# Optimization experiments

Hardware: AMD Instinct MI355X
Metric: run time of the kernel (lower is better)

Reference implementation:

```python
import jax, jax.numpy as jnp
import numpy as np

ROPE_THETA = 500000.0


def apply_rope(x, position_ids):
    # x: (B, H, S, hd), position_ids: (B, S)
    hd = x.shape[-1]
    inv_freq = 1.0 / (ROPE_THETA ** (jnp.arange(0, hd, 2, dtype=x.dtype) / hd))  # (hd/2,)
    freqs = position_ids.astype(x.dtype)[:, :, None] * inv_freq  # (B, S, hd/2)
    sin = jnp.sin(freqs)[:, None, :, :]  # (B, 1, S, hd/2)
    cos = jnp.cos(freqs)[:, None, :, :]
    x1 = x[..., ::2]
    x2 = x[..., 1::2]
    even = x1 * cos - x2 * sin
    odd = x2 * cos + x1 * sin
    # interleave even/odd back: stack on a new trailing axis then flatten
    return jnp.stack([even, odd], axis=-1).reshape(x.shape)


def setup_inputs() -> dict:
    key = jax.random.key(0)
    k_x, k_q, k_k, k_v, k_o = jax.random.split(key, 5)
    B, S, D = 2, 2048, 2048
    H, H_kv = 32, 8
    hd = D // H
    x = jax.random.normal(k_x, (B, S, D), dtype=jnp.float32)
    position_ids = jnp.broadcast_to(jnp.arange(S, dtype=jnp.int64)[None, :], (B, S))
    scale = 0.02
    Wq = jax.random.normal(k_q, (D, H * hd), dtype=jnp.float32) * scale
    Wk = jax.random.normal(k_k, (D, H_kv * hd), dtype=jnp.float32) * scale
    Wv = jax.random.normal(k_v, (D, H_kv * hd), dtype=jnp.float32) * scale
    Wo = jax.random.normal(k_o, (D, D), dtype=jnp.float32) * scale
    return {"x": x, "position_ids": position_ids, "Wq": Wq, "Wk": Wk, "Wv": Wv, "Wo": Wo}


def reference(x, position_ids, Wq, Wk, Wv, Wo):
    B, S, D = x.shape
    H, H_kv = 32, 8
    hd = D // H
    G = H // H_kv  # query heads per kv head

    q = (x @ Wq).reshape(B, S, H, hd).transpose(0, 2, 1, 3)        # (B, H, S, hd)
    k = (x @ Wk).reshape(B, S, H_kv, hd).transpose(0, 2, 1, 3)     # (B, H_kv, S, hd)
    v = (x @ Wv).reshape(B, S, H_kv, hd).transpose(0, 2, 1, 3)

    q = apply_rope(q, position_ids)
    k = apply_rope(k, position_ids)

    # GQA: group query heads (B, H_kv, G, S, hd); repeat_interleave maps head h -> kv head h // G
    qg = q.reshape(B, H_kv, G, S, hd)
    scores = jnp.einsum("bkgsh,bkth->bkgst", qg, k) / jnp.sqrt(jnp.asarray(hd, x.dtype))

    causal = jnp.triu(jnp.ones((S, S), dtype=bool), 1)  # True = masked
    scores = jnp.where(causal, jnp.asarray(-jnp.inf, scores.dtype), scores)

    attn = jax.nn.softmax(scores, axis=-1)  # (B, H_kv, G, S, S)
    z = jnp.einsum("bkgst,bkth->bkgsh", attn, v)  # (B, H_kv, G, S, hd)
    z = z.reshape(B, H, S, hd).transpose(0, 2, 1, 3).reshape(B, S, D)
    return z @ Wo
```

## Files before the change

### kernel.cpp

```cpp
#include <hip/hip_runtime.h>
#include <hip/hip_bf16.h>


#define S_LEN 2048
#define DIM   2048
#define NH    32
#define NKV   8
#define HD    64
#define BS    4096
#define NQKV  3072
#define LL(x) ((long long)(x))

typedef __bf16 bf16x8 __attribute__((ext_vector_type(8)));
typedef float  f32x4  __attribute__((ext_vector_type(4)));
typedef float  f32x16 __attribute__((ext_vector_type(16)));
typedef unsigned u32x4 __attribute__((ext_vector_type(4)));

__device__ __forceinline__ unsigned short bfb(float f) {
  __hip_bfloat16 h = __float2bfloat16(f);
  return *reinterpret_cast<unsigned short*>(&h);
}

__device__ __forceinline__ unsigned cvtpk(float lo, float hi) {
  unsigned u;
  asm("v_cvt_pk_bf16_f32 %0, %1, %2" : "=v"(u) : "v"(lo), "v"(hi));
  return u;
}

__device__ __forceinline__ void gload16(const void* g, void* l) {
  __builtin_amdgcn_global_load_lds(
      (const __attribute__((address_space(1))) void*)g,
      (__attribute__((address_space(3))) void*)l, 16, 0, 0);
}

__device__ __forceinline__ void tcast_body(
    const float* __restrict__ in, unsigned short* __restrict__ out,
    int K, int N, int bx, int by, int tid, float* tile ) {
  int n0 = bx * 32, k0 = by * 32;
  int tx = tid & 31, ty = tid >> 5;
#pragma unroll
  for (int r = 0; r < 32; r += 8)
    tile[(ty + r) * 33 + tx] = in[LL(k0 + ty + r) * N + n0 + tx];
  __syncthreads();
#pragma unroll
  for (int r = 0; r < 32; r += 8)
    out[LL(n0 + ty + r) * K + k0 + tx] = bfb(tile[tx * 33 + ty + r]);
}

__global__ __launch_bounds__(256) void k_prep(
    const float* __restrict__ x,  const float* __restrict__ Wq,
    const float* __restrict__ Wk, const float* __restrict__ Wv,
    const float* __restrict__ Wo, float* __restrict__ tab,
    unsigned short* __restrict__ xb, unsigned short* __restrict__ wqkvt,
    unsigned short* __restrict__ wot) {
  __shared__ float tile[32 * 33];
  int blk = blockIdx.x, tid = threadIdx.x;
  if (blk < 256) {
    int i = blk * 256 + tid;
    int s = i >> 5, f = i & 31;
    double inv = pow(500000.0, -2.0 * (double)f / 64.0);
    double fr = (double)s * inv;
    tab[2 * i]     = (float)cos(fr);
    tab[2 * i + 1] = (float)sin(fr);
  } else if (blk < 8448) {
    int i = (blk - 256) * 256 + tid;
    float4 v = ((const float4*)x)[i];
    ushort4 o;
    o.x = bfb(v.x); o.y = bfb(v.y); o.z = bfb(v.z); o.w = bfb(v.w);
    ((ushort4*)xb)[i] = o;
  } else if (blk < 12544) {
    int t2 = blk - 8448;
    tcast_body(Wq, wqkvt, DIM, DIM, t2 & 63, t2 >> 6, tid, tile);
  } else if (blk < 13568) {
    int t3 = blk - 12544;
    tcast_body(Wk, wqkvt + LL(2048) * DIM, DIM, 512, t3 & 15, t3 >> 4, tid, tile);
  } else if (blk < 14592) {
    int t4 = blk - 13568;
    tcast_body(Wv, wqkvt + LL(2560) * DIM, DIM, 512, t4 & 15, t4 >> 4, tid, tile);
  } else {
    int t5 = blk - 14592;
    tcast_body(Wo, wot, DIM, DIM, t5 & 63, t5 >> 6, tid, tile);
  }
}

template <int MODE>
__global__ __launch_bounds__(256, 2) void k_gemm(
    const unsigned short* __restrict__ A, const unsigned short* __restrict__ Bt,
    void* __restrict__ Cout, int M, int N, int K,
    const float* __restrict__ tab, unsigned short* __restrict__ qbuf,
    unsigned short* __restrict__ kbuf, unsigned short* __restrict__ vtb) {
  __shared__ __align__(16) unsigned short As[128 * 32];
  __shared__ __align__(16) unsigned short Bs[128 * 32];
  int t = threadIdx.x;
  int lane = t & 63, w = t >> 6;
  int wr = w >> 1, wc = w & 1;
  int g = lane >> 4, r = lane & 15;
  int gx = gridDim.x;
  int nwg = gx * gridDim.y;
  int lin = blockIdx.y * gx + blockIdx.x;
  int cpx = nwg >> 3;
  int swz = (lin & 7) * cpx + (lin >> 3);
  int bx = swz % gx, by = swz / gx;
  long long rowBase = LL(by) * 128;
  long long colBase = LL(bx) * 128;

  f32x4 acc[4][4] = {};

  int c0 = t, c1 = t + 256;
  const unsigned short* ag0 = A + (rowBase + (c0 >> 2)) * K + (c0 & 3) * 8;
  const unsigned short* ag1 = A + (rowBase + (c1 >> 2)) * K + (c1 & 3) * 8;
  const unsigned short* bg0 = Bt + (colBase + (c0 >> 2)) * K + (c0 & 3) * 8;
  const unsigned short* bg1 = Bt + (colBase + (c1 >> 2)) * K + (c1 & 3) * 8;
  char* lA0 = (char*)As + c0 * 16; char* lA1 = (char*)As + c1 * 16;
  char* lB0 = (char*)Bs + c0 * 16; char* lB1 = (char*)Bs + c1 * 16;

  for (int kt = 0; kt < K; kt += 32) {
    __syncthreads();
    gload16(ag0 + kt, lA0);
    gload16(ag1 + kt, lA1);
    gload16(bg0 + kt, lB0);
    gload16(bg1 + kt, lB1);
    __syncthreads();

    bf16x8 af[4], bfr[4];
#pragma unroll
    for (int m = 0; m < 4; m++)
      af[m] = *(const bf16x8*)(const void*)(As + (wr * 64 + m * 16 + r) * 32 + g * 8);
#pragma unroll
    for (int n = 0; n < 4; n++)
      bfr[n] = *(const bf16x8*)(const void*)(Bs + (wc * 64 + n * 16 + r) * 32 + g * 8);
#pragma unroll
    for (int m = 0; m < 4; m++)
#pragma unroll
      for (int n = 0; n < 4; n++)
        acc[m][n] = __builtin_amdgcn_mfma_f32_16x16x32_bf16(af[m], bfr[n], acc[m][n], 0, 0, 0);
  }

  if (MODE == 0) {
#pragma unroll
    for (int m = 0; m < 4; m++)
#pragma unroll
      for (int n = 0; n < 4; n++) {
        long long row0 = rowBase + wr * 64 + m * 16 + g * 4;
        long long col = colBase + wc * 64 + n * 16 + r;
#pragma unroll
        for (int j = 0; j < 4; j++)
          ((float*)Cout)[(row0 + j) * N + col] = acc[m][n][j];
      }
  } else {
#pragma unroll
    for (int n = 0; n < 4; n++) {
      int gc0 = (int)colBase + wc * 64 + n * 16;
      int gc = gc0 + r;
      if (gc0 < 2560) {
        unsigned short* dst; int dcol, dstride; float scale;
        if (gc0 < 2048) { dst = qbuf; dcol = gc;        dstride = DIM; scale = 0.18033688f; }
        else            { dst = kbuf; dcol = gc - 2048; dstride = 512; scale = 1.0f; }
        int f = (gc & 63) >> 1;
        float sgn = (gc & 1) ? 1.f : -1.f;
#pragma unroll
        for (int m = 0; m < 4; m++) {
          long long row0 = rowBase + wr * 64 + m * 16 + g * 4;
#pragma unroll
          for (int j = 0; j < 4; j++) {
            float v = acc[m][n][j];
            float part = __shfl_xor(v, 1);
            int s = (int)((row0 + j) & (S_LEN - 1));
            float cc = tab[(s * 32 + f) * 2], ss = tab[(s * 32 + f) * 2 + 1];
            float o = (v * cc + sgn * part * ss) * scale;
            dst[(row0 + j) * dstride + dcol] = bfb(o);
          }
        }
      } else {
        int dcol = gc - 2560;
#pragma unroll
        for (int m = 0; m < 4; m++) {
          long long row0 = rowBase + wr * 64 + m * 16 + g * 4;
#pragma unroll
          for (int j = 0; j < 4; j++) {
            long long row = row0 + j;
            long long bq = row >> 11;
            int s = (int)(row & (S_LEN - 1));
            vtb[(bq * 512 + dcol) * S_LEN + s] = bfb(acc[m][n][j]);
          }
        }
      }
    }
  }
}

__global__ __launch_bounds__(256, 2) void k_attn(
    const unsigned short* __restrict__ qb, const unsigned short* __restrict__ kb,
    const unsigned short* __restrict__ vt, unsigned short* __restrict__ zb) {
  int lin = blockIdx.x + 16 * (blockIdx.y + 32 * blockIdx.z);
  int kvh = lin & 7;
  int idx = lin >> 3;
  int st = 15 - (idx >> 3);
  int b = (idx >> 2) & 1;
  int h = kvh * 4 + (idx & 3);
  int bh = b * NKV + kvh;

  int t = threadIdx.x, lane = t & 63, w = t >> 6;
  int l31 = lane & 31, hi = lane >> 5;
  int sw = (l31 & 7) * 8;

  __shared__ __align__(16) unsigned short Ks[2][64 * 64];
  __shared__ __align__(16) unsigned short Vs[2][64 * 64];

  int c0 = t, c1 = t + 256;
  const unsigned short* kg0 = kb + LL(b) * S_LEN * 512 + (c0 >> 3) * 512 + kvh * HD
                                 + (((c0 & 7) ^ ((c0 >> 3) & 7)) * 8);
  const unsigned short* kg1 = kb + LL(b) * S_LEN * 512 + (c1 >> 3) * 512 + kvh * HD
                                 + (((c1 & 7) ^ ((c1 >> 3) & 7)) * 8);
  const unsigned short* vg0 = vt + (LL(bh) * HD + (c0 >> 3)) * S_LEN
                                 + (((c0 & 7) ^ ((c0 >> 3) & 7)) * 8);
  const unsigned short* vg1 = vt + (LL(bh) * HD + (c1 >> 3)) * S_LEN
                                 + (((c1 & 7) ^ ((c1 >> 3) & 7)) * 8);

#define STAGE(bufi, kst_)                                              \
  {                                                                    \
    gload16(kg0 + LL(kst_) * 512, (char*)Ks[bufi] + c0 * 16);          \
    gload16(kg1 + LL(kst_) * 512, (char*)Ks[bufi] + c1 * 16);          \
    gload16(vg0 + (kst_), (char*)Vs[bufi] + c0 * 16);                  \
    gload16(vg1 + (kst_), (char*)Vs[bufi] + c1 * 16);                  \
  }

  int rowb = st * 128 + w * 32;
  int qg = rowb + l31;
  long long qrow = LL(b) * S_LEN + qg;

  bf16x8 qf[4];
#pragma unroll
  for (int s = 0; s < 4; s++)
    qf[s] = *(const bf16x8*)(const void*)(qb + qrow * DIM + h * HD + s * 16 + hi * 8);

  f32x16 acc0 = {}, acc1 = {};
  float mrun = -1e30f, lrun = 0.f;

  int nt = 2 * st + 2;
  STAGE(0, 0);
  for (int tt = 0; tt < nt; tt++) {
    int kst = tt * 64;
    int cur = tt & 1;
    if (tt + 1 < nt) {
      STAGE(cur ^ 1, kst + 64);
      asm volatile("s_waitcnt vmcnt(4)" ::: "memory");
    } else {
      asm volatile("s_waitcnt vmcnt(0)" ::: "memory");
    }
    __builtin_amdgcn_s_barrier();
    __builtin_amdgcn_sched_barrier(0);

    if (kst <= rowb + 31) {
      const unsigned short* Kc = Ks[cur];
      const unsigned short* Vc = Vs[cur];

      bf16x8 kf[2][4];
#pragma unroll
      for (int kbi = 0; kbi < 2; kbi++)
#pragma unroll
        for (int s = 0; s < 4; s++)
          kf[kbi][s] = *(const bf16x8*)(const void*)(
              Kc + (kbi * 32 + l31) * 64 + ((s * 16 + hi * 8) ^ sw));

      __builtin_amdgcn_s_setprio(1);
      f32x16 sc0 = {}, sc1 = {};
#pragma unroll
      for (int s = 0; s < 4; s++) {
        sc0 = __builtin_amdgcn_mfma_f32_32x32x16_bf16(kf[0][s], qf[s], sc0, 0, 0, 0);
        sc1 = __builtin_amdgcn_mfma_f32_32x32x16_bf16(kf[1][s], qf[s], sc1, 0, 0, 0);
      }
      __builtin_amdgcn_s_setprio(0);

      bf16x8 vf[8];
#pragma unroll
      for (int db = 0; db < 2; db++)
#pragma unroll
        for (int f = 0; f < 4; f++)
          vf[db * 4 + f] = *(const bf16x8*)(const void*)(
              Vc + (db * 32 + l31) * 64 + ((f * 16 + hi * 8) ^ sw));

      if (kst + 63 > rowb) {
#pragma unroll
        for (int q = 0; q < 16; q++) {
          int kl = (q & 3) + 8 * (q >> 2) + 4 * hi;
          if (kst + kl > qg) sc0[q] = -1e30f;
          if (kst + 32 + kl > qg) sc1[q] = -1e30f;
        }
      }

      float pm = -1e30f;
#pragma unroll
      for (int q = 0; q < 16; q++) {
        pm = fmaxf(pm, sc0[q]);
        pm = fmaxf(pm, sc1[q]);
      }
      pm = fmaxf(pm, __shfl_xor(pm, 32));
      if (__any(pm > mrun + 12.0f)) {
        float mnew = fmaxf(mrun, pm);
        float al = exp2f(mrun - mnew);
        mrun = mnew;
        lrun *= al;
        acc0 *= al;
        acc1 *= al;
      }
      f32x16 pv0, pv1;
      float ls = 0.f;
#pragma unroll
      for (int q = 0; q < 16; q++) {
        pv0[q] = exp2f(sc0[q] - mrun);
        pv1[q] = exp2f(sc1[q] - mrun);
        ls += pv0[q] + pv1[q];
      }
      lrun += ls + __shfl_xor(ls, 32);

      bf16x8 pfr[4];
#pragma unroll
      for (int f = 0; f < 4; f++) {
        int qb_ = (f & 1) * 8;
        float e0, e1, e2, e3, e4, e5, e6, e7;
        if (f < 2) {
          e0 = pv0[qb_ + 0]; e1 = pv0[qb_ + 1]; e2 = pv0[qb_ + 2]; e3 = pv0[qb_ + 3];
          e4 = pv0[qb_ + 4]; e5 = pv0[qb_ + 5]; e6 = pv0[qb_ + 6]; e7 = pv0[qb_ + 7];
        } else {
          e0 = pv1[qb_ + 0]; e1 = pv1[qb_ + 1]; e2 = pv1[qb_ + 2]; e3 = pv1[qb_ + 3];
          e4 = pv1[qb_ + 4]; e5 = pv1[qb_ + 5]; e6 = pv1[qb_ + 6]; e7 = pv1[qb_ + 7];
        }
        unsigned a0 = cvtpk(e0, e1), a1 = cvtpk(e2, e3);
        unsigned b0 = cvtpk(e4, e5), b1 = cvtpk(e6, e7);
        unsigned y0 = __shfl_xor(hi ? a0 : b0, 32);
        unsigned y1 = __shfl_xor(hi ? a1 : b1, 32);
        u32x4 uu;
        uu[0] = hi ? y0 : a0;
        uu[1] = hi ? y1 : a1;
        uu[2] = hi ? b0 : y0;
        uu[3] = hi ? b1 : y1;
        pfr[f] = *(bf16x8*)&uu;
      }

      __builtin_amdgcn_s_setprio(1);
#pragma unroll
      for (int f = 0; f < 4; f++) {
        acc0 = __builtin_amdgcn_mfma_f32_32x32x16_bf16(vf[f],     pfr[f], acc0, 0, 0, 0);
        acc1 = __builtin_amdgcn_mfma_f32_32x32x16_bf16(vf[4 + f], pfr[f], acc1, 0, 0, 0);
      }
      __builtin_amdgcn_s_setprio(0);
    }

    __builtin_amdgcn_sched_barrier(0);
    __builtin_amdgcn_s_barrier();
  }

  float invl = 1.0f / lrun;
#pragma unroll
  for (int q4 = 0; q4 < 4; q4++) {
    uint2 u;
    u.x = cvtpk(acc0[q4 * 4 + 0] * invl, acc0[q4 * 4 + 1] * invl);
    u.y = cvtpk(acc0[q4 * 4 + 2] * invl, acc0[q4 * 4 + 3] * invl);
    *(uint2*)(void*)(zb + qrow * DIM + h * HD + 8 * q4 + 4 * hi) = u;
    uint2 v;
    v.x = cvtpk(acc1[q4 * 4 + 0] * invl, acc1[q4 * 4 + 1] * invl);
    v.y = cvtpk(acc1[q4 * 4 + 2] * invl, acc1[q4 * 4 + 3] * invl);
    *(uint2*)(void*)(zb + qrow * DIM + h * HD + 32 + 8 * q4 + 4 * hi) = v;
  }
#undef STAGE
}

extern "C" void kernel_launch(void* const* d_in, const int* in_sizes, int n_in,
                              void* d_out, int out_size, void* d_ws, size_t ws_size,
                              hipStream_t stream) {
  const float* x  = (const float*)d_in[0];
  const float* Wq = (const float*)d_in[2];
  const float* Wk = (const float*)d_in[3];
  const float* Wv = (const float*)d_in[4];
  const float* Wo = (const float*)d_in[5];
  float* out = (float*)d_out;

  char* wsb = (char*)d_ws;
  size_t off = 0;
  auto alloc = [&](size_t bytes) {
    void* p = wsb + off;
    off += (bytes + 255) & ~(size_t)255;
    return p;
  };
  float* tab            = (float*)alloc(LL(S_LEN) * 32 * 2 * 4);
  unsigned short* xb    = (unsigned short*)alloc(LL(BS) * DIM * 2);
  unsigned short* wqkvt = (unsigned short*)alloc(LL(NQKV) * DIM * 2);
  unsigned short* wot   = (unsigned short*)alloc(LL(DIM) * DIM * 2);
  unsigned short* qbuf  = (unsigned short*)alloc(LL(BS) * DIM * 2);
  unsigned short* kbuf  = (unsigned short*)alloc(LL(BS) * (NKV * HD) * 2);
  unsigned short* vtb   = (unsigned short*)alloc(LL(2 * NKV) * HD * S_LEN * 2);
  unsigned short* zb    = (unsigned short*)alloc(LL(BS) * DIM * 2);

  k_prep<<<18688, 256, 0, stream>>>(x, Wq, Wk, Wv, Wo, tab, xb, wqkvt, wot);

  k_gemm<2><<<dim3(NQKV / 128, BS / 128), 256, 0, stream>>>(
      xb, wqkvt, nullptr, BS, NQKV, DIM, tab, qbuf, kbuf, vtb);

  k_attn<<<dim3(16, NH, 2), 256, 0, stream>>>(qbuf, kbuf, vtb, zb);

  k_gemm<0><<<dim3(DIM / 128, BS / 128), 256, 0, stream>>>(
      zb, wot, out, BS, DIM, DIM, nullptr, nullptr, nullptr, nullptr);
}
```

Measured before the change: 198.0 us.

## Split long causal attention tiles across two blocks and merge partials

Query tiles in the upper half of the sequence (st 8..15) now have their KV range split into two halves, each handled by a separate block that writes a normalized partial output plus running max and sum. A new combine kernel merges the two partials with log-sum-exp weights and writes the final bf16 z. The goal is better load balance and shorter tail latency in the causal attention launch, since those tiles were the longest. In exchange it adds an extra kernel launch, extra global traffic for the partial buffers, and a second bf16 rounding of the partial outputs.

```diff
diff --git a/kernel.cpp b/kernel.cpp
--- a/kernel.cpp
+++ b/kernel.cpp
@@ -19,6 +19,10 @@
 __device__ __forceinline__ unsigned short bfb(float f) {
   __hip_bfloat16 h = __float2bfloat16(f);
   return *reinterpret_cast<unsigned short*>(&h);
+}
+
+__device__ __forceinline__ float bf2f(unsigned short u) {
+  return __uint_as_float((unsigned)u << 16);
 }
 
 __device__ __forceinline__ unsigned cvtpk(float lo, float hi) {
@@ -191,13 +195,29 @@
 
 __global__ __launch_bounds__(256, 2) void k_attn(
     const unsigned short* __restrict__ qb, const unsigned short* __restrict__ kb,
-    const unsigned short* __restrict__ vt, unsigned short* __restrict__ zb) {
-  int lin = blockIdx.x + 16 * (blockIdx.y + 32 * blockIdx.z);
+    const unsigned short* __restrict__ vt, unsigned short* __restrict__ zb,
+    unsigned short* __restrict__ obuf, float* __restrict__ mlbuf) {
+  int lin = blockIdx.x;
   int kvh = lin & 7;
-  int idx = lin >> 3;
-  int st = 15 - (idx >> 3);
-  int b = (idx >> 2) & 1;
-  int h = kvh * 4 + (idx & 3);
+  int st, b, hj, half, tt0, tt1;
+  if (lin < 1024) {
+    int s2 = lin >> 3;
+    half = s2 & 1;
+    int rem = s2 >> 1;
+    hj = rem & 3;
+    b = (rem >> 2) & 1;
+    st = 15 - ((rem >> 3) & 7);
+    tt0 = half ? (st + 1) : 0;
+    tt1 = half ? (2 * st + 2) : (st + 1);
+  } else {
+    int u = (lin - 1024) >> 3;
+    hj = u & 3;
+    b = (u >> 2) & 1;
+    st = 7 - ((u >> 3) & 7);
+    half = 0;
+    tt0 = 0; tt1 = 2 * st + 2;
+  }
+  int h = kvh * 4 + hj;
   int bh = b * NKV + kvh;
 
   int t = threadIdx.x, lane = t & 63, w = t >> 6;
@@ -237,12 +257,11 @@
   f32x16 acc0 = {}, acc1 = {};
   float mrun = -1e30f, lrun = 0.f;
 
-  int nt = 2 * st + 2;
-  STAGE(0, 0);
-  for (int tt = 0; tt < nt; tt++) {
+  STAGE(0, tt0 * 64);
+  for (int tt = tt0; tt < tt1; tt++) {
     int kst = tt * 64;
-    int cur = tt & 1;
-    if (tt + 1 < nt) {
+    int cur = (tt - tt0) & 1;
+    if (tt + 1 < tt1) {
       STAGE(cur ^ 1, kst + 64);
       asm volatile("s_waitcnt vmcnt(4)" ::: "memory");
     } else {
@@ -352,18 +371,69 @@
   }
 
   float invl = 1.0f / lrun;
-#pragma unroll
-  for (int q4 = 0; q4 < 4; q4++) {
-    uint2 u;
-    u.x = cvtpk(acc0[q4 * 4 + 0] * invl, acc0[q4 * 4 + 1] * invl);
-    u.y = cvtpk(acc0[q4 * 4 + 2] * invl, acc0[q4 * 4 + 3] * invl);
-    *(uint2*)(void*)(zb + qrow * DIM + h * HD + 8 * q4 + 4 * hi) = u;
-    uint2 v;
-    v.x = cvtpk(acc1[q4 * 4 + 0] * invl, acc1[q4 * 4 + 1] * invl);
-    v.y = cvtpk(acc1[q4 * 4 + 2] * invl, acc1[q4 * 4 + 3] * invl);
-    *(uint2*)(void*)(zb + qrow * DIM + h * HD + 32 + 8 * q4 + 4 * hi) = v;
+  if (lin >= 1024) {
+#pragma unroll
+    for (int q4 = 0; q4 < 4; q4++) {
+      uint2 u;
+      u.x = cvtpk(acc0[q4 * 4 + 0] * invl, acc0[q4 * 4 + 1] * invl);
+      u.y = cvtpk(acc0[q4 * 4 + 2] * invl, acc0[q4 * 4 + 3] * invl);
+      *(uint2*)(void*)(zb + qrow * DIM + h * HD + 8 * q4 + 4 * hi) = u;
+      uint2 v;
+      v.x = cvtpk(acc1[q4 * 4 + 0] * invl, acc1[q4 * 4 + 1] * invl);
+      v.y = cvtpk(acc1[q4 * 4 + 2] * invl, acc1[q4 * 4 + 3] * invl);
+      *(uint2*)(void*)(zb + qrow * DIM + h * HD + 32 + 8 * q4 + 4 * hi) = v;
+    }
+  } else {
+    int grp2 = ((b * 32 + h) * 8 + (st - 8)) * 2 + half;
+    unsigned short* ob = obuf + LL(grp2) * 8192;
+    int row = w * 32 + l31;
+#pragma unroll
+    for (int q4 = 0; q4 < 4; q4++) {
+#pragma unroll
+      for (int jj = 0; jj < 4; jj++) {
+        int d0 = 8 * q4 + 4 * hi + jj;
+        ob[d0 * 128 + row]        = bfb(acc0[q4 * 4 + jj] * invl);
+        ob[(d0 + 32) * 128 + row] = bfb(acc1[q4 * 4 + jj] * invl);
+      }
+    }
+    if (hi == 0) {
+      mlbuf[grp2 * 256 + row] = mrun;
+      mlbuf[grp2 * 256 + 128 + row] = lrun;
+    }
   }
 #undef STAGE
+}
+
+__global__ __launch_bounds__(256) void k_comb(
+    const unsigned short* __restrict__ obuf, const float* __restrict__ mlbuf,
+    unsigned short* __restrict__ zb) {
+  int g = blockIdx.x;
+  int st = 8 + (g & 7);
+  int bh = g >> 3;
+  int h = bh & 31, b = bh >> 5;
+  int t = threadIdx.x;
+  int row = t >> 1;
+  int dbase = (t & 1) * 32;
+  const unsigned short* o0 = obuf + LL(g) * 2 * 8192;
+  const unsigned short* o1 = o0 + 8192;
+  float m0 = mlbuf[(g * 2 + 0) * 256 + row];
+  float l0 = mlbuf[(g * 2 + 0) * 256 + 128 + row];
+  float m1 = mlbuf[(g * 2 + 1) * 256 + row];
+  float l1 = mlbuf[(g * 2 + 1) * 256 + 128 + row];
+  float m = fmaxf(m0, m1);
+  float w0 = l0 * exp2f(m0 - m);
+  float w1 = l1 * exp2f(m1 - m);
+  float inv = 1.0f / (w0 + w1);
+  w0 *= inv; w1 *= inv;
+  long long zoff = (LL(b) * S_LEN + st * 128 + row) * DIM + h * HD + dbase;
+#pragma unroll
+  for (int d = 0; d < 32; d += 2) {
+    float f0 = bf2f(o0[(dbase + d) * 128 + row]) * w0
+             + bf2f(o1[(dbase + d) * 128 + row]) * w1;
+    float f1 = bf2f(o0[(dbase + d + 1) * 128 + row]) * w0
+             + bf2f(o1[(dbase + d + 1) * 128 + row]) * w1;
+    *(unsigned*)(void*)(zb + zoff + d) = cvtpk(f0, f1);
+  }
 }
 
 extern "C" void kernel_launch(void* const* d_in, const int* in_sizes, int n_in,
@@ -391,13 +461,17 @@
   unsigned short* kbuf  = (unsigned short*)alloc(LL(BS) * (NKV * HD) * 2);
   unsigned short* vtb   = (unsigned short*)alloc(LL(2 * NKV) * HD * S_LEN * 2);
   unsigned short* zb    = (unsigned short*)alloc(LL(BS) * DIM * 2);
+  unsigned short* obuf  = (unsigned short*)alloc(LL(1024) * 8192 * 2);
+  float* mlbuf          = (float*)alloc(LL(1024) * 256 * 4);
 
   k_prep<<<18688, 256, 0, stream>>>(x, Wq, Wk, Wv, Wo, tab, xb, wqkvt, wot);
 
   k_gemm<2><<<dim3(NQKV / 128, BS / 128), 256, 0, stream>>>(
       xb, wqkvt, nullptr, BS, NQKV, DIM, tab, qbuf, kbuf, vtb);
 
-  k_attn<<<dim3(16, NH, 2), 256, 0, stream>>>(qbuf, kbuf, vtb, zb);
+  k_attn<<<1536, 256, 0, stream>>>(qbuf, kbuf, vtb, zb, obuf, mlbuf);
+
+  k_comb<<<512, 256, 0, stream>>>(obuf, mlbuf, zb);
 
   k_gemm<0><<<dim3(DIM / 128, BS / 128), 256, 0, stream>>>(
       zb, wot, out, BS, DIM, DIM, nullptr, nullptr, nullptr, nullptr);
```

Result: slower. 211.7 us (+6.9%).
